# Performance work log

Measured on AMD Instinct MI355X. Metric: run time of the kernel, lower is better.

Reference implementation:

```python
import jax, jax.numpy as jnp
import numpy as np

DIM = 512
HEADS = 8
DIM_HEAD = 64
INNER = HEADS * DIM_HEAD  # 512
NARROW_K = 9
WIDE_K = 9
WIDE_DIL = 5


def setup_inputs() -> dict:
    key = jax.random.key(0)
    ks = jax.random.split(key, 12)
    b, n = 4, 2048
    s = lambda fan_in: 1.0 / np.sqrt(fan_in)
    inp = {
        'tokens': jax.random.normal(ks[0], (b, n, DIM), jnp.float32),
        'mask': jax.random.randint(ks[1], (b, n), 0, 2) > 0,
        'w_qkv': jax.random.normal(ks[2], (DIM, INNER * 3), jnp.float32) * s(DIM),
        'w_out': jax.random.normal(ks[3], (INNER, DIM), jnp.float32) * s(INNER),
        'b_out': jnp.zeros((DIM,), jnp.float32),
        'w_narrow': jax.random.normal(ks[4], (DIM, DIM, NARROW_K), jnp.float32) * s(DIM * NARROW_K),
        'b_narrow': jnp.zeros((DIM,), jnp.float32),
        'w_wide': jax.random.normal(ks[5], (DIM, DIM, WIDE_K), jnp.float32) * s(DIM * WIDE_K),
        'b_wide': jnp.zeros((DIM,), jnp.float32),
        'ln1_g': jnp.ones((DIM,), jnp.float32),
        'ln1_b': jnp.zeros((DIM,), jnp.float32),
        'ff_w': jax.random.normal(ks[6], (DIM, DIM), jnp.float32) * s(DIM),
        'ff_b': jnp.zeros((DIM,), jnp.float32),
        'ln2_g': jnp.ones((DIM,), jnp.float32),
        'ln2_b': jnp.zeros((DIM,), jnp.float32),
    }
    return inp


def layer_norm(x, g, b, eps=1e-5):
    m = jnp.mean(x, axis=-1, keepdims=True)
    v = jnp.mean(jnp.square(x - m), axis=-1, keepdims=True)
    return (x - m) / jnp.sqrt(v + eps) * g + b


def rope_encoding(seq_len, dim_head, dtype):
    inv_freq = 1.0 / (10000.0 ** (jnp.arange(0, dim_head, 2, dtype=jnp.float32) / dim_head))
    pos = jnp.arange(seq_len, dtype=jnp.float32)
    sinu = jnp.einsum('i,j->ij', pos, inv_freq)  # [n, d/2]
    return jnp.concatenate([jnp.sin(sinu), jnp.cos(sinu)], axis=-1).astype(dtype)  # [n, d]


def attn(tokens, mask, w_qkv, w_out, b_out):
    b, n, _ = tokens.shape
    qkv = tokens @ w_qkv  # [b, n, 3*inner]
    q, k, v = jnp.split(qkv, 3, axis=-1)
    reshp = lambda t: t.reshape(b, n, HEADS, DIM_HEAD).transpose(0, 2, 1, 3)  # b h n d
    q, k, v = reshp(q), reshp(k), reshp(v)
    rope = rope_encoding(n, DIM_HEAD, tokens.dtype)  # [n, d]
    q = q + rope
    k = k + rope
    mask4 = mask[:, None, :, None]  # b 1 n 1
    big = jnp.finfo(k.dtype).max
    k = jnp.where(mask4, k, -big)
    q = jax.nn.softmax(q, axis=-1) * (DIM_HEAD ** -0.5)
    k = jax.nn.softmax(k, axis=2)  # over n
    v = jnp.where(mask4, v, 0.0)
    context = jnp.einsum('bhnd,bhne->bhde', k, v)
    out = jnp.einsum('bhde,bhnd->bhne', context, q)
    out = out.transpose(0, 2, 1, 3).reshape(b, n, INNER)
    return out @ w_out + b_out


def conv1d(x, w, b, padding, dilation):
    # x: [b, c, n], w: [out, in, k]
    y = jax.lax.conv_general_dilated(
        x, w, window_strides=(1,), padding=[(padding, padding)],
        rhs_dilation=(dilation,), dimension_numbers=('NCW', 'OIW', 'NCW'))
    return y + b[None, :, None]


def reference(tokens, mask, w_qkv, w_out, b_out, w_narrow, b_narrow,
              w_wide, b_wide, ln1_g, ln1_b, ff_w, ff_b, ln2_g, ln2_b):
    tokens = attn(tokens, mask, w_qkv, w_out, b_out)
    conv_in = tokens.transpose(0, 2, 1)  # b d n
    conv_in = jnp.where(mask[:, None, :], conv_in, 0.0)
    narrow = jax.nn.gelu(conv1d(conv_in, w_narrow, b_narrow, NARROW_K // 2, 1), approximate=False)
    wide_pad = (WIDE_K + (WIDE_K - 1) * (WIDE_DIL - 1)) // 2  # 20
    wide = jax.nn.gelu(conv1d(conv_in, w_wide, b_wide, wide_pad, WIDE_DIL), approximate=False)
    tokens = tokens + narrow.transpose(0, 2, 1) + wide.transpose(0, 2, 1)
    tokens = layer_norm(tokens, ln1_g, ln1_b)
    tokens = layer_norm(jax.nn.gelu(tokens @ ff_w + ff_b, approximate=False), ln2_g, ln2_b)
    return tokens
```

## Files before the change

kernel.cpp:

```cpp
#include <hip/hip_runtime.h>
#include <hip/hip_bf16.h>

#define BB 4
#define NN 2048
#define NROWS (BB*NN)

typedef unsigned short u16;
typedef __bf16 bf16x8 __attribute__((ext_vector_type(8)));
typedef u16    u16x8  __attribute__((ext_vector_type(8)));
typedef u16    u16x2  __attribute__((ext_vector_type(2)));
typedef float  fx4    __attribute__((ext_vector_type(4)));

__device__ __forceinline__ float bf2f(u16 u){
  union { float f; unsigned int i; } x; x.i = ((unsigned int)u) << 16; return x.f;
}
__device__ __forceinline__ u16 f2bf(float f){
  union { float f; unsigned int i; } x; x.f = f;
  unsigned int i = x.i;
  i += 0x7fffu + ((i >> 16) & 1u);
  return (u16)(i >> 16);
}
__device__ __forceinline__ float geluf(float x){
  return 0.5f * x * (1.0f + erff(x * 0.70710678118654752f));
}
__device__ __forceinline__ void gload16(const void* g, void* l){
  __builtin_amdgcn_global_load_lds((const __attribute__((address_space(1))) unsigned int*)g,
                                   (__attribute__((address_space(3))) unsigned int*)l, 16, 0, 0);
}

__global__ __launch_bounds__(256) void sniff_k(const u16* tokens, const unsigned int* mask, int* flags){
  __shared__ int s_f32, s_byte;
  if (threadIdx.x == 0) { s_f32 = 0; s_byte = 0; }
  __syncthreads();
  for (int i = threadIdx.x; i < 4096; i += 256) {
    float v = bf2f(tokens[i]);
    if (!(fabsf(v) < 1e10f)) atomicOr(&s_f32, 1);
  }
  for (int i = threadIdx.x; i < 2048; i += 256) {
    if (mask[i] > 1u) atomicOr(&s_byte, 1);
  }
  __syncthreads();
  if (threadIdx.x == 0) { flags[0] = s_f32; flags[1] = s_byte; }
}

__global__ __launch_bounds__(256) void misc_k(const void* mask, const void* tokens,
                                              const void* p0, const void* p1, const void* p2,
                                              const void* p3, const void* p4, const void* p5,
                                              const void* p6, const void* p7,
                                              const int* flags, float* rope, int* m32,
                                              float* params, float* ctx, float* kS, u16* tokbf){
  const void* srcs[8] = {p0,p1,p2,p3,p4,p5,p6,p7};
  int f32 = flags[0], mbyte = flags[1];
  const int T = 131072 + 8192 + 4096 + 131072 + 2048 + 4194304;
  for (int i = blockIdx.x*256 + threadIdx.x; i < T; i += gridDim.x*256) {
    if (i < 131072) {
      int p = i >> 6, j = i & 63;
      int jj = (j < 32) ? j : j - 32;
      float invf = exp2f(-(float)jj * (13.287712379549449f/32.0f));
      float prod = (float)p * invf;
      rope[i] = (j < 32) ? sinf(prod) : cosf(prod);
    } else if (i < 139264) {
      int k = i - 131072;
      int v = mbyte ? (int)((const unsigned char*)mask)[k] : ((const int*)mask)[k];
      m32[k] = v ? 1 : 0;
    } else if (i < 143360) {
      int k = i - 139264;
      int pid = k >> 9, j = k & 511;
      const void* s = srcs[pid];
      params[k] = f32 ? ((const float*)s)[j] : bf2f(((const u16*)s)[j]);
    } else if (i < 274432) {
      ctx[i - 143360] = 0.0f;
    } else if (i < 276480) {
      kS[i - 274432] = 0.0f;
    } else {
      int k = i - 276480;
      tokbf[k] = f32 ? f2bf(((const float*)tokens)[k]) : ((const u16*)tokens)[k];
    }
  }
}

__global__ __launch_bounds__(256) void prep2_k(const void* w_qkv, const void* w_out, const void* ff_w,
                                               const void* w_narrow, const void* w_wide,
                                               const int* flags,
                                               u16* wqkvt, u16* woutt, u16* ffwt,
                                               u16* wtN2, u16* wtW2){
  int bid = blockIdx.x;
  int f = flags[0];
  int tid = threadIdx.x;
  if (bid < 1024) {
    int tensor = bid >> 9, o = bid & 511;
    const void* src = tensor ? w_wide : w_narrow;
    u16* dst = tensor ? wtW2 : wtN2;
    __shared__ u16 Ls[4608];
    for (int i = tid; i < 4608; i += 256) {
      Ls[i] = f ? f2bf(((const float*)src)[(size_t)o*4608 + i]) : ((const u16*)src)[(size_t)o*4608 + i];
    }
    __syncthreads();
    #pragma unroll
    for (int kk = 0; kk < 9; kk++) {
      #pragma unroll
      for (int u = 0; u < 2; u++) {
        int c = tid + u*256;
        dst[(size_t)kk*262144 + o*512 + c] = Ls[c*9 + kk];
      }
    }
  } else {
    int id = bid - 1024;
    int z = id / 192;
    int rem = id - z*192;
    int x = rem % 24, y = rem / 24;
    int Nn = (z == 0) ? 1536 : 512;
    if (x * 64 >= Nn) return;
    const void* src = (z == 0) ? w_qkv : (z == 1) ? w_out : ff_w;
    u16* dst = (z == 0) ? wqkvt : (z == 1) ? woutt : ffwt;
    __shared__ u16 Ts[64][72];
    int n0 = x * 64, k0 = y * 64;
    int r = tid >> 2, cq = (tid & 3) * 16;
    #pragma unroll
    for (int u = 0; u < 2; u++) {
      int c = cq + u*8;
      int sidx = (k0 + r)*Nn + n0 + c;
      u16x8 v;
      if (f) {
        #pragma unroll
        for (int j = 0; j < 8; j++) v[j] = f2bf(((const float*)src)[sidx + j]);
      } else {
        v = *(const u16x8*)&((const u16*)src)[sidx];
      }
      *(u16x8*)&Ts[r][c] = v;
    }
    __syncthreads();
    #pragma unroll
    for (int u = 0; u < 2; u++) {
      int c = cq + u*8;
      u16x8 v;
      #pragma unroll
      for (int j = 0; j < 8; j++) v[j] = Ts[c + j][r];
      *(u16x8*)&dst[(size_t)(n0 + r)*512 + k0 + c] = v;
    }
  }
}

__global__ __launch_bounds__(256) void mgemm_qkv_k(const u16* A, const u16* Bt, const float* rope,
                                                   const int* mask, u16* qb, u16* keb, u16* vb){
  __shared__ u16 As[128*32];
  __shared__ u16 Bs[128*32];
  __shared__ int smask[128];
  int tid = threadIdx.x;
  int lane = tid & 63;
  int wave = tid >> 6;
  int wm = (wave >> 1) * 64, wn = (wave & 1) * 64;
  int quad = lane >> 4, l16 = lane & 15;
  int m0 = blockIdx.y * 128, n0 = blockIdx.x * 128;
  fx4 acc[4][4] = {};
  for (int k0 = 0; k0 < 512; k0 += 32) {
    #pragma unroll
    for (int it = 0; it < 2; it++) {
      int s = it*256 + tid;
      int lsl = ((s & 3) ^ ((s >> 3) & 3)) * 8;
      gload16(&A[(size_t)(m0 + (s >> 2))*512 + k0 + lsl], &As[(it*256 + wave*64)*8]);
    }
    #pragma unroll
    for (int it = 0; it < 2; it++) {
      int s = it*256 + tid;
      int lsl = ((s & 3) ^ ((s >> 3) & 3)) * 8;
      gload16(&Bt[(size_t)(n0 + (s >> 2))*512 + k0 + lsl], &Bs[(it*256 + wave*64)*8]);
    }
    __syncthreads();
    bf16x8 af[4], bfv[4];
    #pragma unroll
    for (int i = 0; i < 4; i++) {
      int row = wm + i*16 + l16;
      af[i] = __builtin_bit_cast(bf16x8,
                *(const u16x8*)&As[row*32 + ((quad ^ ((row >> 1) & 3)) * 8)]);
    }
    #pragma unroll
    for (int j = 0; j < 4; j++) {
      int row = wn + j*16 + l16;
      bfv[j] = __builtin_bit_cast(bf16x8,
                *(const u16x8*)&Bs[row*32 + ((quad ^ ((row >> 1) & 3)) * 8)]);
    }
    #pragma unroll
    for (int i = 0; i < 4; i++)
      #pragma unroll
      for (int j = 0; j < 4; j++)
        acc[i][j] = __builtin_amdgcn_mfma_f32_16x16x32_bf16(af[i], bfv[j], acc[i][j], 0, 0, 0);
    __syncthreads();
  }
  int x = blockIdx.x;
  if (x >= 4) {
    if (tid < 128) smask[tid] = mask[m0 + tid];
    __syncthreads();
  }
  if (x < 4) {
    #pragma unroll
    for (int i = 0; i < 4; i++)
      #pragma unroll
      for (int r = 0; r < 4; r++) {
        int rl = wm + i*16 + quad*4 + r;
        int row = m0 + rl;
        int nseq = row & (NN-1);
        const float* rp = rope + nseq*64 + l16;
        float e0 = __expf(acc[i][0][r] + rp[0]);
        float e1 = __expf(acc[i][1][r] + rp[16]);
        float e2 = __expf(acc[i][2][r] + rp[32]);
        float e3 = __expf(acc[i][3][r] + rp[48]);
        float s = e0 + e1 + e2 + e3;
        s += __shfl_xor(s, 1); s += __shfl_xor(s, 2);
        s += __shfl_xor(s, 4); s += __shfl_xor(s, 8);
        float sc = 0.125f / s;
        size_t base = (size_t)row*512 + n0 + wn + l16;
        qb[base]      = f2bf(e0*sc);
        qb[base + 16] = f2bf(e1*sc);
        qb[base + 32] = f2bf(e2*sc);
        qb[base + 48] = f2bf(e3*sc);
      }
  } else if (x < 8) {
    #pragma unroll
    for (int i = 0; i < 4; i++)
      #pragma unroll
      for (int r = 0; r < 4; r++) {
        int rl = wm + i*16 + quad*4 + r;
        int row = m0 + rl;
        int nseq = row & (NN-1);
        int mk = smask[rl];
        const float* rp = rope + nseq*64 + l16;
        size_t base = (size_t)row*512 + (n0 - 512) + wn + l16;
        #pragma unroll
        for (int j = 0; j < 4; j++) {
          float ke = mk ? __expf(acc[i][j][r] + rp[j*16]) : 0.0f;
          keb[base + j*16] = f2bf(ke);
        }
      }
  } else {
    #pragma unroll
    for (int i = 0; i < 4; i++)
      #pragma unroll
      for (int r = 0; r < 4; r++) {
        int rl = wm + i*16 + quad*4 + r;
        int row = m0 + rl;
        int mk = smask[rl];
        size_t base = (size_t)row*512 + (n0 - 1024) + wn + l16;
        #pragma unroll
        for (int j = 0; j < 4; j++)
          vb[base + j*16] = mk ? f2bf(acc[i][j][r]) : (u16)0;
      }
  }
}

#define FMA16(a, b, acc) \
  acc[0][0] = fmaf(a.x, b.x, acc[0][0]); acc[0][1] = fmaf(a.x, b.y, acc[0][1]); \
  acc[0][2] = fmaf(a.x, b.z, acc[0][2]); acc[0][3] = fmaf(a.x, b.w, acc[0][3]); \
  acc[1][0] = fmaf(a.y, b.x, acc[1][0]); acc[1][1] = fmaf(a.y, b.y, acc[1][1]); \
  acc[1][2] = fmaf(a.y, b.z, acc[1][2]); acc[1][3] = fmaf(a.y, b.w, acc[1][3]); \
  acc[2][0] = fmaf(a.z, b.x, acc[2][0]); acc[2][1] = fmaf(a.z, b.y, acc[2][1]); \
  acc[2][2] = fmaf(a.z, b.z, acc[2][2]); acc[2][3] = fmaf(a.z, b.w, acc[2][3]); \
  acc[3][0] = fmaf(a.w, b.x, acc[3][0]); acc[3][1] = fmaf(a.w, b.y, acc[3][1]); \
  acc[3][2] = fmaf(a.w, b.z, acc[3][2]); acc[3][3] = fmaf(a.w, b.w, acc[3][3]);

__global__ __launch_bounds__(256) void ctx_k(const u16* keb, const u16* vb, float* ctx, float* Sg){
  int bh = blockIdx.x, seg = blockIdx.y;
  int b = bh >> 3, h = bh & 7;
  __shared__ float Ks[32][68], Vs[32][68];
  __shared__ float sS[64];
  int tid = threadIdx.x, tx = tid & 15, ty = tid >> 4;
  if (tid < 64) sS[tid] = 0.0f;
  float acc[4][4] = {{0.f,0.f,0.f,0.f},{0.f,0.f,0.f,0.f},{0.f,0.f,0.f,0.f},{0.f,0.f,0.f,0.f}};
  float sp[8] = {0,0,0,0,0,0,0,0};
  int nl = tid >> 3, dcol = (tid & 7)*8;
  const u16* kp0 = keb + (size_t)(b*NN + seg*256)*512 + h*64 + dcol;
  const u16* vp0 = vb  + (size_t)(b*NN + seg*256)*512 + h*64 + dcol;
  for (int nc = 0; nc < 256; nc += 32) {
    u16x8 ku = *(const u16x8*)(kp0 + (size_t)(nc + nl)*512);
    u16x8 vu = *(const u16x8*)(vp0 + (size_t)(nc + nl)*512);
    float a[8], bb[8];
    #pragma unroll
    for (int t = 0; t < 8; t++) { a[t] = bf2f(ku[t]); bb[t] = bf2f(vu[t]); sp[t] += a[t]; }
    *(float4*)&Ks[nl][dcol]   = (float4){a[0],a[1],a[2],a[3]};
    *(float4*)&Ks[nl][dcol+4] = (float4){a[4],a[5],a[6],a[7]};
    *(float4*)&Vs[nl][dcol]   = (float4){bb[0],bb[1],bb[2],bb[3]};
    *(float4*)&Vs[nl][dcol+4] = (float4){bb[4],bb[5],bb[6],bb[7]};
    __syncthreads();
    #pragma unroll
    for (int q = 0; q < 32; q++) {
      float4 a4 = *(const float4*)&Ks[q][ty*4];
      float4 b4 = *(const float4*)&Vs[q][tx*4];
      FMA16(a4, b4, acc)
    }
    __syncthreads();
  }
  #pragma unroll
  for (int j = 0; j < 8; j++) atomicAdd(&sS[dcol + j], sp[j]);
  float* cp = ctx + (size_t)bh*4096;
  #pragma unroll
  for (int i = 0; i < 4; i++)
    #pragma unroll
    for (int j = 0; j < 4; j++)
      atomicAdd(&cp[(ty*4 + i)*64 + tx*4 + j], acc[i][j]);
  __syncthreads();
  if (tid < 64) atomicAdd(&Sg[bh*64 + tid], sS[tid]);
}

__global__ __launch_bounds__(256) void ctxw_k(const float* ctx, const float* Sg, const u16* woutt,
                                              u16* W2t, u16* cpadb){
  int bx = blockIdx.x;
  int tid = threadIdx.x;
  if (bx >= 32) {
    int idx = (bx - 32)*256 + tid;
    if (idx < BB*40*512) {
      int c = idx & 511;
      int t = (idx >> 9) % 40;
      int b = idx / (40*512);
      int tt = (t < 20) ? t : 2048 + t;
      cpadb[((size_t)b*2088 + tt)*512 + c] = 0;
    }
    return;
  }
  int h = bx & 7, b = bx >> 3;
  int lane = tid & 63, wave = tid >> 6;
  int quad = lane >> 4, l16 = lane & 15;
  const float* cp = ctx + (size_t)(b*8 + h)*4096;
  fx4 acc[8][4] = {};
  #pragma unroll
  for (int ks = 0; ks < 2; ks++) {
    bf16x8 bfv[4];
    #pragma unroll
    for (int j = 0; j < 4; j++) {
      int d = j*16 + l16;
      float S = Sg[(b*8 + h)*64 + d];
      float rs = (S > 0.0f) ? 1.0f/S : 0.0f;
      const float* src = cp + d*64 + ks*32 + quad*8;
      float4 v0 = *(const float4*)src, v1 = *(const float4*)(src + 4);
      bf16x8 t;
      t[0]=(__bf16)(v0.x*rs); t[1]=(__bf16)(v0.y*rs); t[2]=(__bf16)(v0.z*rs); t[3]=(__bf16)(v0.w*rs);
      t[4]=(__bf16)(v1.x*rs); t[5]=(__bf16)(v1.y*rs); t[6]=(__bf16)(v1.z*rs); t[7]=(__bf16)(v1.w*rs);
      bfv[j] = t;
    }
    #pragma unroll
    for (int i = 0; i < 8; i++) {
      int orow = wave*128 + i*16 + l16;
      bf16x8 afr = __builtin_bit_cast(bf16x8, *(const u16x8*)&woutt[(size_t)orow*512 + h*64 + ks*32 + quad*8]);
      #pragma unroll
      for (int j = 0; j < 4; j++)
        acc[i][j] = __builtin_amdgcn_mfma_f32_16x16x32_bf16(afr, bfv[j], acc[i][j], 0, 0, 0);
    }
  }
  u16* out = W2t + (size_t)b*262144;
  #pragma unroll
  for (int i = 0; i < 8; i++)
    #pragma unroll
    for (int j = 0; j < 4; j++)
      #pragma unroll
      for (int r = 0; r < 4; r++) {
        int orow = wave*128 + i*16 + quad*4 + r;
        out[(size_t)orow*512 + h*64 + j*16 + l16] = f2bf(acc[i][j][r]);
      }
}

__global__ __launch_bounds__(256) void mgemm_attn64_k(const u16* qb, const u16* W2t, const float* bias,
                                                      const int* mask, u16* attnb, u16* cpadb){
  __shared__ u16 As[64][40];
  __shared__ u16 Bs[128][40];
  int tid = threadIdx.x;
  int lane = tid & 63;
  int wave = tid >> 6;
  int wn = wave * 32;
  int quad = lane >> 4, l16 = lane & 15;
  int m0 = blockIdx.y * 64, n0 = blockIdx.x * 128, b = blockIdx.z;
  const u16* A  = qb  + (size_t)b*2048*512;
  const u16* Bt = W2t + (size_t)b*262144;
  fx4 acc[4][2] = {};
  int ar = tid >> 2;
  int ac = (tid & 3) * 8;
  for (int k0 = 0; k0 < 512; k0 += 32) {
    *(u16x8*)&As[ar][ac]    = *(const u16x8*)&A[(size_t)(m0+ar)*512 + k0 + ac];
    *(u16x8*)&Bs[ar][ac]    = *(const u16x8*)&Bt[(size_t)(n0+ar)*512 + k0 + ac];
    *(u16x8*)&Bs[ar+64][ac] = *(const u16x8*)&Bt[(size_t)(n0+ar+64)*512 + k0 + ac];
    __syncthreads();
    bf16x8 af[4], bfv[2];
    #pragma unroll
    for (int i = 0; i < 4; i++)
      af[i] = __builtin_bit_cast(bf16x8, *(const u16x8*)&As[i*16 + l16][quad*8]);
    #pragma unroll
    for (int j = 0; j < 2; j++)
      bfv[j] = __builtin_bit_cast(bf16x8, *(const u16x8*)&Bs[wn + j*16 + l16][quad*8]);
    #pragma unroll
    for (int i = 0; i < 4; i++)
      #pragma unroll
      for (int j = 0; j < 2; j++)
        acc[i][j] = __builtin_amdgcn_mfma_f32_16x16x32_bf16(af[i], bfv[j], acc[i][j], 0, 0, 0);
    __syncthreads();
  }
  #pragma unroll
  for (int i = 0; i < 4; i++)
    #pragma unroll
    for (int j = 0; j < 2; j++) {
      int col = n0 + wn + j*16 + l16;
      float bv = bias[col];
      #pragma unroll
      for (int r = 0; r < 4; r++) {
        int row_l = m0 + i*16 + quad*4 + r;
        float v = acc[i][j][r] + bv;
        u16 vbb = f2bf(v);
        attnb[((size_t)b*2048 + row_l)*512 + col] = vbb;
        int mk = mask[b*2048 + row_l];
        cpadb[((size_t)b*2088 + row_l + 20)*512 + col] = mk ? vbb : (u16)0;
      }
    }
}

#define A_ROWS 552
#define A_SZ (A_ROWS*32)
#define W_SZ (9*64*32)
__global__ __launch_bounds__(512, 2) void mconv13_k(const u16* cpad, const u16* Wn, const u16* Ww,
                                                    const float* bias_n, const float* bias_w,
                                                    u16* Dn, u16* Dw){
  __shared__ u16 As[2*A_SZ];
  __shared__ u16 Ws[2*W_SZ];
  int tid = threadIdx.x;
  int lane = tid & 63;
  int wave = tid >> 6;
  int wm = wave * 64;
  int quad = lane >> 4, l16 = lane & 15;
  int o0 = blockIdx.x * 64, m0 = blockIdx.y * 512;
  int b = blockIdx.z >> 1, cid = blockIdx.z & 1;
  const u16* W = cid ? Ww : Wn;
  const float* bias = cid ? bias_w : bias_n;
  u16* D = cid ? Dw : Dn;
  fx4 acc[4][4] = {};
  const u16* cb = cpad + ((size_t)b*2088 + m0)*512;
  int wslot = ((quad ^ ((l16 >> 1) & 3)) * 8);
  int sbase = cid ? 0 : 16;
  int sstep = cid ? 5 : 1;
  int rowb0 = sbase + wm + l16;

#define STAGE_CHUNK(c0, buf)                                                          \
  {                                                                                   \
    _Pragma("unroll")                                                                 \
    for (int it = 0; it < 5; it++) {                                                  \
      int s = it*512 + tid;                                                           \
      if (s < 2208) {                                                                 \
        int lsl = ((s & 3) ^ ((s >> 3) & 3)) * 8;                                     \
        gload16(&cb[(size_t)(s >> 2)*512 + (c0) + lsl],                               \
                &As[(buf)*A_SZ + (it*512 + wave*64)*8]);                              \
      }                                                                               \
    }                                                                                 \
    _Pragma("unroll")                                                                 \
    for (int it = 0; it < 5; it++) {                                                  \
      int s = it*512 + tid;                                                           \
      if (s < 2304) {                                                                 \
        int kk = s >> 8;                                                              \
        int ow = (s >> 2) & 63;                                                       \
        int lsl = ((s & 3) ^ ((s >> 3) & 3)) * 8;                                     \
        gload16(&W[(size_t)kk*262144 + (size_t)(o0 + ow)*512 + (c0) + lsl],           \
                &Ws[(buf)*W_SZ + (it*512 + wave*64)*8]);                              \
      }                                                                               \
    }                                                                                 \
  }

#define LOADFRAG(kk, bfv, afr)                                                        \
  {                                                                                   \
    int rowb = rowb0 + sstep*(kk);                                                    \
    int aslot = ((quad ^ ((rowb >> 1) & 3)) * 8);                                     \
    _Pragma("unroll")                                                                 \
    for (int j = 0; j < 4; j++)                                                       \
      bfv[j] = __builtin_bit_cast(bf16x8,                                             \
                 *(const u16x8*)&Wsb[((kk)*64 + j*16 + l16)*32 + wslot]);             \
    _Pragma("unroll")                                                                 \
    for (int i = 0; i < 4; i++)                                                       \
      afr[i] = __builtin_bit_cast(bf16x8,                                             \
                 *(const u16x8*)&Asb[(rowb + i*16)*32 + aslot]);                      \
  }

#define MFMATAP_SGB(bfv, afr)                                                         \
  {                                                                                   \
    _Pragma("unroll")                                                                 \
    for (int i = 0; i < 4; i++)                                                       \
      _Pragma("unroll")                                                               \
      for (int j = 0; j < 4; j++)                                                     \
        acc[i][j] = __builtin_amdgcn_mfma_f32_16x16x32_bf16(afr[i], bfv[j],           \
                                                            acc[i][j], 0, 0, 0);      \
    _Pragma("unroll")                                                                 \
    for (int g = 0; g < 8; g++) {                                                     \
      __builtin_amdgcn_sched_group_barrier(0x008, 2, 0);                  \
      __builtin_amdgcn_sched_group_barrier(0x100, 1, 0);               \
    }                                                                                 \
  }

#define MFMATAP_PLAIN(bfv, afr)                                                       \
  {                                                                                   \
    _Pragma("unroll")                                                                 \
    for (int i = 0; i < 4; i++)                                                       \
      _Pragma("unroll")                                                               \
      for (int j = 0; j < 4; j++)                                                     \
        acc[i][j] = __builtin_amdgcn_mfma_f32_16x16x32_bf16(afr[i], bfv[j],           \
                                                            acc[i][j], 0, 0, 0);      \
  }

  STAGE_CHUNK(0, 0)
  __syncthreads();

  for (int ch = 0; ch < 16; ch++) {
    int cur = ch & 1;
    const u16* Asb = &As[cur*A_SZ];
    const u16* Wsb = &Ws[cur*W_SZ];
    bf16x8 bfvA[4], afrA[4], bfvB[4], afrB[4];
    LOADFRAG(0, bfvA, afrA)
    if (ch < 15) {
      int c0n = (ch + 1) * 32;
      int nb = cur ^ 1;
      STAGE_CHUNK(c0n, nb)
    }
    #pragma unroll
    for (int kt = 0; kt < 8; kt += 2) {
      LOADFRAG(kt+1, bfvB, afrB)
      MFMATAP_SGB(bfvA, afrA)
      LOADFRAG(kt+2, bfvA, afrA)
      MFMATAP_SGB(bfvB, afrB)
    }
    MFMATAP_PLAIN(bfvA, afrA)
    __syncthreads();
  }
#undef STAGE_CHUNK
#undef LOADFRAG
#undef MFMATAP_SGB
#undef MFMATAP_PLAIN
  #pragma unroll
  for (int i = 0; i < 4; i++)
    #pragma unroll
    for (int j = 0; j < 4; j++) {
      int col = o0 + j*16 + l16;
      float bv = bias[col];
      #pragma unroll
      for (int r = 0; r < 4; r++) {
        int row = b*2048 + m0 + wm + i*16 + quad*4 + r;
        D[(size_t)row*512 + col] = f2bf(geluf(acc[i][j][r] + bv));
      }
    }
}

template<bool BIAS, bool GELU>
__global__ __launch_bounds__(256) void mgemm64b_k(const u16* A, const u16* Bt, const float* bias,
                                                  u16* C, int M, int N, int K){
  __shared__ u16 As[64][40];
  __shared__ u16 Bs[128][40];
  int tid = threadIdx.x;
  int lane = tid & 63;
  int wave = tid >> 6;
  int wn = wave * 32;
  int quad = lane >> 4, l16 = lane & 15;
  int m0 = blockIdx.y * 64, n0 = blockIdx.x * 128;
  fx4 acc[4][2] = {};
  int ar = tid >> 2;
  int ac = (tid & 3) * 8;
  for (int k0 = 0; k0 < K; k0 += 32) {
    *(u16x8*)&As[ar][ac]    = *(const u16x8*)&A[(size_t)(m0+ar)*K + k0 + ac];
    *(u16x8*)&Bs[ar][ac]    = *(const u16x8*)&Bt[(size_t)(n0+ar)*K + k0 + ac];
    *(u16x8*)&Bs[ar+64][ac] = *(const u16x8*)&Bt[(size_t)(n0+ar+64)*K + k0 + ac];
    __syncthreads();
    bf16x8 af[4], bfv[2];
    #pragma unroll
    for (int i = 0; i < 4; i++)
      af[i] = __builtin_bit_cast(bf16x8, *(const u16x8*)&As[i*16 + l16][quad*8]);
    #pragma unroll
    for (int j = 0; j < 2; j++)
      bfv[j] = __builtin_bit_cast(bf16x8, *(const u16x8*)&Bs[wn + j*16 + l16][quad*8]);
    #pragma unroll
    for (int i = 0; i < 4; i++)
      #pragma unroll
      for (int j = 0; j < 2; j++)
        acc[i][j] = __builtin_amdgcn_mfma_f32_16x16x32_bf16(af[i], bfv[j], acc[i][j], 0, 0, 0);
    __syncthreads();
  }
  #pragma unroll
  for (int i = 0; i < 4; i++)
    #pragma unroll
    for (int j = 0; j < 2; j++) {
      int col = n0 + wn + j*16 + l16;
      float bv = BIAS ? bias[col] : 0.0f;
      #pragma unroll
      for (int r = 0; r < 4; r++) {
        int row = m0 + i*16 + quad*4 + r;
        float v = acc[i][j][r] + bv;
        if (GELU) v = geluf(v);
        C[(size_t)row*N + col] = f2bf(v);
      }
    }
}

__device__ __forceinline__ float block_sum512(float v, float* red){
  #pragma unroll
  for (int o = 32; o; o >>= 1) v += __shfl_xor(v, o, 64);
  int w = threadIdx.x >> 6;
  if ((threadIdx.x & 63) == 0) red[w] = v;
  __syncthreads();
  float t = red[0] + red[1] + red[2] + red[3];
  __syncthreads();
  return t;
}

template<int NADD, int OM>
__global__ __launch_bounds__(256) void ln_k(const u16* X, const u16* Y, const u16* Z,
                                            const float* g, const float* be,
                                            const int* flags, void* out){
  __shared__ float red[4];
  size_t row = blockIdx.x;
  int tid = threadIdx.x;
  int c = tid * 2;
  u16x2 xv = *(const u16x2*)&X[row*512 + c];
  float x0 = bf2f(xv[0]), x1 = bf2f(xv[1]);
  if (NADD >= 1) { u16x2 yv = *(const u16x2*)&Y[row*512 + c]; x0 += bf2f(yv[0]); x1 += bf2f(yv[1]); }
  if (NADD >= 2) { u16x2 zv = *(const u16x2*)&Z[row*512 + c]; x0 += bf2f(zv[0]); x1 += bf2f(zv[1]); }
  float mean = block_sum512(x0 + x1, red) * (1.0f/512.0f);
  float d0 = x0 - mean, d1 = x1 - mean;
  float var = block_sum512(d0*d0 + d1*d1, red) * (1.0f/512.0f);
  float inv = rsqrtf(var + 1e-5f);
  float2 gv = *(const float2*)&g[c];
  float2 bv = *(const float2*)&be[c];
  float r0 = d0*inv*gv.x + bv.x;
  float r1 = d1*inv*gv.y + bv.y;
  bool obf = (OM == 1) || (OM == 2 && !flags[0]);
  if (obf) {
    u16x2 ov; ov[0] = f2bf(r0); ov[1] = f2bf(r1);
    *(u16x2*)&((u16*)out)[row*512 + c] = ov;
  } else {
    float2 ov; ov.x = r0; ov.y = r1;
    *(float2*)&((float*)out)[row*512 + c] = ov;
  }
}

extern "C" void kernel_launch(void* const* d_in, const int* in_sizes, int n_in,
                              void* d_out, int out_size, void* d_ws, size_t ws_size,
                              hipStream_t stream) {
  const void* tokens   = d_in[0];
  const void* mask     = d_in[1];
  const void* w_qkv    = d_in[2];
  const void* w_out    = d_in[3];
  const void* b_out    = d_in[4];
  const void* w_narrow = d_in[5];
  const void* b_narrow = d_in[6];
  const void* w_wide   = d_in[7];
  const void* b_wide   = d_in[8];
  const void* ln1_g    = d_in[9];
  const void* ln1_b    = d_in[10];
  const void* ff_w     = d_in[11];
  const void* ff_b     = d_in[12];
  const void* ln2_g    = d_in[13];
  const void* ln2_b    = d_in[14];

  float* ws = (float*)d_ws;
  int*   flags  = (int*)ws;
  int*   m32    = (int*)(ws + 16);
  float* params = ws + 8208;
  float* kS     = ws + 12304;
  float* ctx    = ws + 14352;
  float* rope   = ws + 145424;
  u16*   tokbf  = (u16*)(ws + 276496);
  u16*   wqkvt  = (u16*)(ws + 2373648);
  u16*   woutt  = (u16*)(ws + 2766864);
  u16*   ffwt   = (u16*)(ws + 2897936);
  u16*   wtN2   = (u16*)(ws + 3029008);
  u16*   wtW2   = (u16*)(ws + 4208656);
  u16*   qb     = (u16*)(ws + 5388304);
  u16*   keb    = (u16*)(ws + 7485456);
  u16*   vb     = (u16*)(ws + 9582608);
  u16*   W2t    = (u16*)(ws + 11679760);
  u16*   attnb  = (u16*)(ws + 12204048);
  u16*   cpadb  = (u16*)(ws + 14301200);
  u16*   Dnb    = (u16*)(ws + 16439312);
  u16*   Dwb    = (u16*)(ws + 18536464);
  u16*   Eb     = attnb;
  u16*   t1b    = tokbf;

  float* p_bout = params;        float* p_bnar = params + 512;
  float* p_bwid = params + 1024; float* p_l1g  = params + 1536;
  float* p_l1b  = params + 2048; float* p_ffb  = params + 2560;
  float* p_l2g  = params + 3072; float* p_l2b  = params + 3584;

  sniff_k<<<dim3(1), dim3(256), 0, stream>>>((const u16*)tokens, (const unsigned int*)mask, flags);
  misc_k<<<dim3(8192), dim3(256), 0, stream>>>(mask, tokens, b_out, b_narrow, b_wide, ln1_g, ln1_b,
                                               ff_b, ln2_g, ln2_b, flags, rope, m32, params, ctx,
                                               kS, tokbf);
  prep2_k<<<dim3(1600), dim3(256), 0, stream>>>(w_qkv, w_out, ff_w, w_narrow, w_wide, flags,
                                                wqkvt, woutt, ffwt, wtN2, wtW2);

  mgemm_qkv_k<<<dim3(12, 64), dim3(256), 0, stream>>>(
      tokbf, wqkvt, rope, m32, qb, keb, vb);

  ctx_k<<<dim3(32, 8), dim3(256), 0, stream>>>(keb, vb, ctx, kS);

  ctxw_k<<<dim3(352), dim3(256), 0, stream>>>(ctx, kS, woutt, W2t, cpadb);

  mgemm_attn64_k<<<dim3(4, 32, 4), dim3(256), 0, stream>>>(qb, W2t, p_bout, m32, attnb, cpadb);

  mconv13_k<<<dim3(8, 4, 8), dim3(512), 0, stream>>>(cpadb, wtN2, wtW2, p_bnar, p_bwid, Dnb, Dwb);

  ln_k<2,1><<<dim3(NROWS), dim3(256), 0, stream>>>(attnb, Dnb, Dwb, p_l1g, p_l1b, flags, (void*)t1b);

  mgemm64b_k<true,true><<<dim3(4, 128), dim3(256), 0, stream>>>(
      t1b, ffwt, p_ffb, Eb, NROWS, 512, 512);

  ln_k<0,2><<<dim3(NROWS), dim3(256), 0, stream>>>(Eb, nullptr, nullptr, p_l2g, p_l2b, flags, d_out);
}
```

Baseline: 327.5 us.

## Merge prep kernels, precompute conv load addresses, retile FF GEMM to 128x128

Fuses the misc and weight-transpose prep kernels into a single launch, which removes one kernel launch and its tail. In the conv kernel, global load pointers and validity predicates are computed once before the loop instead of per chunk, reducing integer address arithmetic. The feed-forward GEMM moves from 64x128 tiles with 256 threads to 128x128 tiles with 512 threads, using direct global-to-LDS loads and a swizzled LDS layout. The larger tiles give more reuse but halve the block count and raise register and LDS pressure.

```diff
diff --git a/kernel.cpp b/kernel.cpp
--- a/kernel.cpp
+++ b/kernel.cpp
@@ -43,52 +43,51 @@
   if (threadIdx.x == 0) { flags[0] = s_f32; flags[1] = s_byte; }
 }
 
-__global__ __launch_bounds__(256) void misc_k(const void* mask, const void* tokens,
-                                              const void* p0, const void* p1, const void* p2,
-                                              const void* p3, const void* p4, const void* p5,
-                                              const void* p6, const void* p7,
-                                              const int* flags, float* rope, int* m32,
-                                              float* params, float* ctx, float* kS, u16* tokbf){
-  const void* srcs[8] = {p0,p1,p2,p3,p4,p5,p6,p7};
-  int f32 = flags[0], mbyte = flags[1];
-  const int T = 131072 + 8192 + 4096 + 131072 + 2048 + 4194304;
-  for (int i = blockIdx.x*256 + threadIdx.x; i < T; i += gridDim.x*256) {
-    if (i < 131072) {
-      int p = i >> 6, j = i & 63;
-      int jj = (j < 32) ? j : j - 32;
-      float invf = exp2f(-(float)jj * (13.287712379549449f/32.0f));
-      float prod = (float)p * invf;
-      rope[i] = (j < 32) ? sinf(prod) : cosf(prod);
-    } else if (i < 139264) {
-      int k = i - 131072;
-      int v = mbyte ? (int)((const unsigned char*)mask)[k] : ((const int*)mask)[k];
-      m32[k] = v ? 1 : 0;
-    } else if (i < 143360) {
-      int k = i - 139264;
-      int pid = k >> 9, j = k & 511;
-      const void* s = srcs[pid];
-      params[k] = f32 ? ((const float*)s)[j] : bf2f(((const u16*)s)[j]);
-    } else if (i < 274432) {
-      ctx[i - 143360] = 0.0f;
-    } else if (i < 276480) {
-      kS[i - 274432] = 0.0f;
-    } else {
-      int k = i - 276480;
-      tokbf[k] = f32 ? f2bf(((const float*)tokens)[k]) : ((const u16*)tokens)[k];
-    }
-  }
-}
-
-__global__ __launch_bounds__(256) void prep2_k(const void* w_qkv, const void* w_out, const void* ff_w,
+__global__ __launch_bounds__(256) void misc2_k(const void* mask, const void* tokens,
+                                               const void* p0, const void* p1, const void* p2,
+                                               const void* p3, const void* p4, const void* p5,
+                                               const void* p6, const void* p7,
+                                               const int* flags, float* rope, int* m32,
+                                               float* params, float* ctx, float* kS, u16* tokbf,
+                                               const void* w_qkv, const void* w_out, const void* ff_w,
                                                const void* w_narrow, const void* w_wide,
-                                               const int* flags,
                                                u16* wqkvt, u16* woutt, u16* ffwt,
                                                u16* wtN2, u16* wtW2){
   int bid = blockIdx.x;
+  int tid = threadIdx.x;
   int f = flags[0];
-  int tid = threadIdx.x;
-  if (bid < 1024) {
-    int tensor = bid >> 9, o = bid & 511;
+  if (bid < 8192) {
+    const void* srcs[8] = {p0,p1,p2,p3,p4,p5,p6,p7};
+    int mbyte = flags[1];
+    const int T = 131072 + 8192 + 4096 + 131072 + 2048 + 4194304;
+    for (int i = bid*256 + tid; i < T; i += 8192*256) {
+      if (i < 131072) {
+        int p = i >> 6, j = i & 63;
+        int jj = (j < 32) ? j : j - 32;
+        float invf = exp2f(-(float)jj * (13.287712379549449f/32.0f));
+        float prod = (float)p * invf;
+        rope[i] = (j < 32) ? sinf(prod) : cosf(prod);
+      } else if (i < 139264) {
+        int k = i - 131072;
+        int v = mbyte ? (int)((const unsigned char*)mask)[k] : ((const int*)mask)[k];
+        m32[k] = v ? 1 : 0;
+      } else if (i < 143360) {
+        int k = i - 139264;
+        int pid = k >> 9, j = k & 511;
+        const void* s = srcs[pid];
+        params[k] = f ? ((const float*)s)[j] : bf2f(((const u16*)s)[j]);
+      } else if (i < 274432) {
+        ctx[i - 143360] = 0.0f;
+      } else if (i < 276480) {
+        kS[i - 274432] = 0.0f;
+      } else {
+        int k = i - 276480;
+        tokbf[k] = f ? f2bf(((const float*)tokens)[k]) : ((const u16*)tokens)[k];
+      }
+    }
+  } else if (bid < 9216) {
+    int id = bid - 8192;
+    int tensor = id >> 9, o = id & 511;
     const void* src = tensor ? w_wide : w_narrow;
     u16* dst = tensor ? wtW2 : wtN2;
     __shared__ u16 Ls[4608];
@@ -105,7 +104,7 @@
       }
     }
   } else {
-    int id = bid - 1024;
+    int id = bid - 9216;
     int z = id / 192;
     int rem = id - z*192;
     int x = rem % 24, y = rem / 24;
@@ -412,7 +411,7 @@
 #define A_ROWS 552
 #define A_SZ (A_ROWS*32)
 #define W_SZ (9*64*32)
-__global__ __launch_bounds__(512, 2) void mconv13_k(const u16* cpad, const u16* Wn, const u16* Ww,
+__global__ __launch_bounds__(512, 2) void mconv15_k(const u16* cpad, const u16* Wn, const u16* Ww,
                                                     const float* bias_n, const float* bias_w,
                                                     u16* Dn, u16* Dw){
   __shared__ u16 As[2*A_SZ];
@@ -434,27 +433,37 @@
   int sstep = cid ? 5 : 1;
   int rowb0 = sbase + wm + l16;
 
+  const u16* ap[5]; bool av[5];
+  #pragma unroll
+  for (int it = 0; it < 5; it++) {
+    int s = it*512 + tid;
+    av[it] = (s < 2208);
+    int row = av[it] ? (s >> 2) : 0;
+    int lsl = ((s & 3) ^ ((s >> 3) & 3)) * 8;
+    ap[it] = cb + (size_t)row*512 + lsl;
+  }
+  const u16* wp[5]; bool wv[5];
+  #pragma unroll
+  for (int it = 0; it < 5; it++) {
+    int s = it*512 + tid;
+    wv[it] = (s < 2304);
+    int kk = wv[it] ? (s >> 8) : 0;
+    int ow = (s >> 2) & 63;
+    int lsl = ((s & 3) ^ ((s >> 3) & 3)) * 8;
+    wp[it] = W + (size_t)kk*262144 + (size_t)(o0 + ow)*512 + lsl;
+  }
+
 #define STAGE_CHUNK(c0, buf)                                                          \
   {                                                                                   \
     _Pragma("unroll")                                                                 \
     for (int it = 0; it < 5; it++) {                                                  \
-      int s = it*512 + tid;                                                           \
-      if (s < 2208) {                                                                 \
-        int lsl = ((s & 3) ^ ((s >> 3) & 3)) * 8;                                     \
-        gload16(&cb[(size_t)(s >> 2)*512 + (c0) + lsl],                               \
-                &As[(buf)*A_SZ + (it*512 + wave*64)*8]);                              \
-      }                                                                               \
+      if (av[it])                                                                     \
+        gload16(ap[it] + (c0), &As[(buf)*A_SZ + (it*512 + wave*64)*8]);               \
     }                                                                                 \
     _Pragma("unroll")                                                                 \
     for (int it = 0; it < 5; it++) {                                                  \
-      int s = it*512 + tid;                                                           \
-      if (s < 2304) {                                                                 \
-        int kk = s >> 8;                                                              \
-        int ow = (s >> 2) & 63;                                                       \
-        int lsl = ((s & 3) ^ ((s >> 3) & 3)) * 8;                                     \
-        gload16(&W[(size_t)kk*262144 + (size_t)(o0 + ow)*512 + (c0) + lsl],           \
-                &Ws[(buf)*W_SZ + (it*512 + wave*64)*8]);                              \
-      }                                                                               \
+      if (wv[it])                                                                     \
+        gload16(wp[it] + (c0), &Ws[(buf)*W_SZ + (it*512 + wave*64)*8]);               \
     }                                                                                 \
   }
 
@@ -539,32 +548,43 @@
     }
 }
 
-template<bool BIAS, bool GELU>
-__global__ __launch_bounds__(256) void mgemm64b_k(const u16* A, const u16* Bt, const float* bias,
-                                                  u16* C, int M, int N, int K){
-  __shared__ u16 As[64][40];
-  __shared__ u16 Bs[128][40];
+__global__ __launch_bounds__(512) void mgemm128b_k(const u16* A, const u16* Bt, const float* bias,
+                                                   u16* C){
+  __shared__ u16 As[128*32];
+  __shared__ u16 Bs[128*32];
   int tid = threadIdx.x;
   int lane = tid & 63;
   int wave = tid >> 6;
-  int wn = wave * 32;
+  int wm = (wave >> 2) * 64;
+  int wn = (wave & 3) * 32;
   int quad = lane >> 4, l16 = lane & 15;
-  int m0 = blockIdx.y * 64, n0 = blockIdx.x * 128;
+  int m0 = blockIdx.y * 128, n0 = blockIdx.x * 128;
   fx4 acc[4][2] = {};
-  int ar = tid >> 2;
-  int ac = (tid & 3) * 8;
-  for (int k0 = 0; k0 < K; k0 += 32) {
-    *(u16x8*)&As[ar][ac]    = *(const u16x8*)&A[(size_t)(m0+ar)*K + k0 + ac];
-    *(u16x8*)&Bs[ar][ac]    = *(const u16x8*)&Bt[(size_t)(n0+ar)*K + k0 + ac];
-    *(u16x8*)&Bs[ar+64][ac] = *(const u16x8*)&Bt[(size_t)(n0+ar+64)*K + k0 + ac];
+  for (int k0 = 0; k0 < 512; k0 += 32) {
+    {
+      int s = tid;
+      int lsl = ((s & 3) ^ ((s >> 3) & 3)) * 8;
+      gload16(&A[(size_t)(m0 + (s >> 2))*512 + k0 + lsl], &As[(wave*64)*8]);
+    }
+    {
+      int s = tid;
+      int lsl = ((s & 3) ^ ((s >> 3) & 3)) * 8;
+      gload16(&Bt[(size_t)(n0 + (s >> 2))*512 + k0 + lsl], &Bs[(wave*64)*8]);
+    }
     __syncthreads();
     bf16x8 af[4], bfv[2];
     #pragma unroll
-    for (int i = 0; i < 4; i++)
-      af[i] = __builtin_bit_cast(bf16x8, *(const u16x8*)&As[i*16 + l16][quad*8]);
-    #pragma unroll
-    for (int j = 0; j < 2; j++)
-      bfv[j] = __builtin_bit_cast(bf16x8, *(const u16x8*)&Bs[wn + j*16 + l16][quad*8]);
+    for (int i = 0; i < 4; i++) {
+      int row = wm + i*16 + l16;
+      af[i] = __builtin_bit_cast(bf16x8,
+                *(const u16x8*)&As[row*32 + ((quad ^ ((row >> 1) & 3)) * 8)]);
+    }
+    #pragma unroll
+    for (int j = 0; j < 2; j++) {
+      int row = wn + j*16 + l16;
+      bfv[j] = __builtin_bit_cast(bf16x8,
+                *(const u16x8*)&Bs[row*32 + ((quad ^ ((row >> 1) & 3)) * 8)]);
+    }
     #pragma unroll
     for (int i = 0; i < 4; i++)
       #pragma unroll
@@ -577,13 +597,11 @@
     #pragma unroll
     for (int j = 0; j < 2; j++) {
       int col = n0 + wn + j*16 + l16;
-      float bv = BIAS ? bias[col] : 0.0f;
+      float bv = bias[col];
       #pragma unroll
       for (int r = 0; r < 4; r++) {
-        int row = m0 + i*16 + quad*4 + r;
-        float v = acc[i][j][r] + bv;
-        if (GELU) v = geluf(v);
-        C[(size_t)row*N + col] = f2bf(v);
+        int row = m0 + wm + i*16 + quad*4 + r;
+        C[(size_t)row*512 + col] = f2bf(geluf(acc[i][j][r] + bv));
       }
     }
 }
@@ -678,10 +696,10 @@
   float* p_l2g  = params + 3072; float* p_l2b  = params + 3584;
 
   sniff_k<<<dim3(1), dim3(256), 0, stream>>>((const u16*)tokens, (const unsigned int*)mask, flags);
-  misc_k<<<dim3(8192), dim3(256), 0, stream>>>(mask, tokens, b_out, b_narrow, b_wide, ln1_g, ln1_b,
-                                               ff_b, ln2_g, ln2_b, flags, rope, m32, params, ctx,
-                                               kS, tokbf);
-  prep2_k<<<dim3(1600), dim3(256), 0, stream>>>(w_qkv, w_out, ff_w, w_narrow, w_wide, flags,
+
+  misc2_k<<<dim3(9792), dim3(256), 0, stream>>>(mask, tokens, b_out, b_narrow, b_wide, ln1_g, ln1_b,
+                                                ff_b, ln2_g, ln2_b, flags, rope, m32, params, ctx,
+                                                kS, tokbf, w_qkv, w_out, ff_w, w_narrow, w_wide,
                                                 wqkvt, woutt, ffwt, wtN2, wtW2);
 
   mgemm_qkv_k<<<dim3(12, 64), dim3(256), 0, stream>>>(
@@ -693,12 +711,11 @@
 
   mgemm_attn64_k<<<dim3(4, 32, 4), dim3(256), 0, stream>>>(qb, W2t, p_bout, m32, attnb, cpadb);
 
-  mconv13_k<<<dim3(8, 4, 8), dim3(512), 0, stream>>>(cpadb, wtN2, wtW2, p_bnar, p_bwid, Dnb, Dwb);
+  mconv15_k<<<dim3(8, 4, 8), dim3(512), 0, stream>>>(cpadb, wtN2, wtW2, p_bnar, p_bwid, Dnb, Dwb);
 
   ln_k<2,1><<<dim3(NROWS), dim3(256), 0, stream>>>(attnb, Dnb, Dwb, p_l1g, p_l1b, flags, (void*)t1b);
 
-  mgemm64b_k<true,true><<<dim3(4, 128), dim3(256), 0, stream>>>(
-      t1b, ffwt, p_ffb, Eb, NROWS, 512, 512);
+  mgemm128b_k<<<dim3(4, 64), dim3(512), 0, stream>>>(t1b, ffwt, p_ffb, Eb);
 
   ln_k<0,2><<<dim3(NROWS), dim3(256), 0, stream>>>(Eb, nullptr, nullptr, p_l2g, p_l2b, flags, d_out);
 }
```

Measured after the change: 321.9 us. Within noise of the previous version (-1.7%).
